# Performance work log

Hardware: AMD Instinct MI355X
Metric: run time of the kernel (lower is better)

Reference implementation:

```python
import jax, jax.numpy as jnp
import numpy as np

N_NODES = 100000
N_EDGES = 1200000
D_IN = 256
D_OUT = 64


def setup_inputs() -> dict:
    key = jax.random.key(0)
    k1, k2, k3, k4, k5 = jax.random.split(key, 5)
    x = jax.random.normal(k1, (N_NODES, D_IN), dtype=jnp.float32)
    edge_row = jax.random.randint(k2, (N_EDGES,), 0, N_NODES, dtype=jnp.int64)
    edge_col = jax.random.randint(k3, (N_EDGES,), 0, N_NODES, dtype=jnp.int64)
    edge_val = jax.random.uniform(k4, (N_EDGES,), dtype=jnp.float32)
    # Xavier-uniform weight, as in reset_parameters()
    limit = float(np.sqrt(6.0 / (D_IN + D_OUT)))
    weight = jax.random.uniform(k5, (D_IN, D_OUT), dtype=jnp.float32,
                                minval=-limit, maxval=limit)
    return {"x": x, "edge_row": edge_row, "edge_col": edge_col,
            "edge_val": edge_val, "weight": weight}


def reference(x, edge_row, edge_col, edge_val, weight):
    # eval mode / dropout p=0.0 -> dropout is identity
    support = x @ weight                               # [N, D_OUT] dense GEMM
    # sparse adjacency spmm: out[i] = sum_{e: row[e]==i} val[e] * support[col[e]]
    msgs = edge_val[:, None] * support[edge_col]       # [E, D_OUT] gather
    out = jax.ops.segment_sum(msgs, edge_row, num_segments=N_NODES)  # scatter-add
    return jax.nn.relu(out)
```

## Files before the change

kernel.cpp:

```cpp
#include <hip/hip_runtime.h>
#include <hip/hip_bf16.h>

#define N_NODES 100000
#define N_EDGES 1200000
#define D_IN 256
#define D_OUT 64
#define N_TILES (N_NODES / 16)

#define NG 1280
#define FUSED_NB (NG * 2)
#define EDGE4_NB ((N_EDGES / 4 + 255) / 256)

#define FILL_PASSES 2
#define PASS_NODES (N_NODES / FILL_PASSES)
#define FILL_NB ((N_EDGES / 4 + 255) / 256)

#define SCAN_BLOCK 1024
#define SCAN_NB ((N_NODES + SCAN_BLOCK - 1) / SCAN_BLOCK)

typedef __bf16 bf16_t;
typedef bf16_t bf16x8 __attribute__((ext_vector_type(8)));
typedef float f32x4 __attribute__((ext_vector_type(4)));

__device__ __forceinline__ unsigned pack_cv(int col, float val) {
    return ((unsigned)col << 15) | (unsigned)(val * 32767.f + 0.5f);
}

__device__ __forceinline__ bf16x8 cvt8(float4 lo, float4 hi) {
    bf16x8 a;
    a[0] = (bf16_t)lo.x; a[1] = (bf16_t)lo.y;
    a[2] = (bf16_t)lo.z; a[3] = (bf16_t)lo.w;
    a[4] = (bf16_t)hi.x; a[5] = (bf16_t)hi.y;
    a[6] = (bf16_t)hi.z; a[7] = (bf16_t)hi.w;
    return a;
}

__device__ __forceinline__ void gld_lds16(const void* g, void* l) {
    __builtin_amdgcn_global_load_lds(
        (const __attribute__((address_space(1))) void*)g,
        (__attribute__((address_space(3))) void*)l, 16, 0, 0);
}

__global__ __launch_bounds__(256) void pack_w(const float* __restrict__ W,
                                              bf16_t* __restrict__ Wpack) {
    int id = blockIdx.x * 256 + threadIdx.x;
    if (id < D_IN * D_OUT) {
        int i  = id & 7;
        int l  = (id >> 3) & 63;
        int n  = (id >> 9) & 3;
        int kk = id >> 11;
        int k = kk * 32 + (l >> 4) * 8 + i;
        int c = n * 16 + (l & 15);
        Wpack[id] = (bf16_t)W[k * D_OUT + c];
    }
}

__device__ __forceinline__ void stage_tile(const char* __restrict__ xtile,
                                           char* ldsbuf, int wave, int lane) {
#pragma unroll
    for (int i = 0; i < 4; ++i) {
        int kk = i * 2 + (wave >> 1);
        const char* src = xtile + (lane & 15) * 1024 + (lane >> 4) * 32
                        + kk * 128 + (wave & 1) * 16;
        gld_lds16(src, ldsbuf + i * 4096 + wave * 1024);
    }
}

__device__ __forceinline__ void compute_store(const char* buf,
                                              const bf16x8* wf,
                                              int lane, int lrow, int g, int wave,
                                              bf16_t* __restrict__ support,
                                              int tile) {
    f32x4 acc = {0.f, 0.f, 0.f, 0.f};
#pragma unroll
    for (int kk = 0; kk < 8; ++kk) {
        float4 lo = *(const float4*)(buf + kk * 2048 + lane * 16);
        float4 hi = *(const float4*)(buf + kk * 2048 + 1024 + lane * 16);
        acc = __builtin_amdgcn_mfma_f32_16x16x32_bf16(cvt8(lo, hi), wf[kk],
                                                      acc, 0, 0, 0);
    }
    bf16_t* __restrict__ sp = support + (size_t)tile * 16 * D_OUT
                            + wave * 16 + lrow;
#pragma unroll
    for (int q = 0; q < 4; ++q)
        sp[(g * 4 + q) * D_OUT] = (bf16_t)acc[q];
}

__global__ __launch_bounds__(256, 5) void gemm_hist_cv(
        const float* __restrict__ x, const bf16x8* __restrict__ Wpack,
        bf16_t* __restrict__ support,
        const int* __restrict__ erow, const int* __restrict__ ecol,
        const float* __restrict__ eval,
        int* __restrict__ counts, unsigned* __restrict__ rcv) {
    __shared__ char xlds[2][16384];
    int bid  = blockIdx.x;
    int role = bid & 1;
    int idx  = bid >> 1;
    if (role == 0) {
        int lane = threadIdx.x & 63;
        int wave = threadIdx.x >> 6;
        int lrow = lane & 15;
        int g    = lane >> 4;

        bf16x8 wf[8];
#pragma unroll
        for (int kk = 0; kk < 8; ++kk)
            wf[kk] = Wpack[(kk * 4 + wave) * 64 + lane];

        const char* xc = (const char*)x;
        int t = idx;
        stage_tile(xc + (size_t)t * 16384, xlds[0], wave, lane);

        int cur = 0;
#pragma unroll 1
        for (; t < N_TILES; t += NG) {
            int nxt = t + NG;
            if (nxt < N_TILES) {
                stage_tile(xc + (size_t)nxt * 16384, xlds[cur ^ 1], wave, lane);
                if (t == idx) {
                    asm volatile("s_waitcnt vmcnt(4)" ::: "memory");
                } else {
                    asm volatile("s_waitcnt vmcnt(8)" ::: "memory");
                }
            } else {
                asm volatile("s_waitcnt vmcnt(4)" ::: "memory");
            }
            __builtin_amdgcn_s_barrier();
            __builtin_amdgcn_sched_barrier(0);
            compute_store(xlds[cur], wf, lane, lrow, g, wave, support, t);
            __builtin_amdgcn_s_barrier();
            __builtin_amdgcn_sched_barrier(0);
            cur ^= 1;
        }
    } else {
        if (idx >= EDGE4_NB) return;
        int e = (idx * 256 + threadIdx.x) * 4;
        if (e + 3 < N_EDGES) {
            int4   r4 = *(const int4*)(erow + e);
            int4   c4 = *(const int4*)(ecol + e);
            float4 v4 = *(const float4*)(eval + e);
            unsigned p0 = (unsigned)atomicAdd(&counts[r4.x], 1);
            unsigned p1 = (unsigned)atomicAdd(&counts[r4.y], 1);
            unsigned p2 = (unsigned)atomicAdd(&counts[r4.z], 1);
            unsigned p3 = (unsigned)atomicAdd(&counts[r4.w], 1);
            uint4 o1, o2;
            o1.x = pack_cv(c4.x, v4.x); o1.y = (unsigned)r4.x | (p0 << 17);
            o1.z = pack_cv(c4.y, v4.y); o1.w = (unsigned)r4.y | (p1 << 17);
            o2.x = pack_cv(c4.z, v4.z); o2.y = (unsigned)r4.z | (p2 << 17);
            o2.z = pack_cv(c4.w, v4.w); o2.w = (unsigned)r4.w | (p3 << 17);
            *(uint4*)(rcv + 2 * e)     = o1;
            *(uint4*)(rcv + 2 * e + 4) = o2;
        } else {
            for (int i = 0; i < 4; ++i) {
                if (e + i < N_EDGES) {
                    int rr = erow[e + i];
                    unsigned pp = (unsigned)atomicAdd(&counts[rr], 1);
                    rcv[2 * (e + i)]     = pack_cv(ecol[e + i], eval[e + i]);
                    rcv[2 * (e + i) + 1] = (unsigned)rr | (pp << 17);
                }
            }
        }
    }
}

__global__ __launch_bounds__(256) void partial_k(const int* __restrict__ counts,
                                                 int* __restrict__ bsum) {
    int b = blockIdx.x, t = threadIdx.x;
    int base = b * SCAN_BLOCK + t * 4;
    int s = 0;
    if (base + 3 < N_NODES) {
        int4 v = *(const int4*)(counts + base);
        s = ((v.x + 3) & ~3) + ((v.y + 3) & ~3) + ((v.z + 3) & ~3) + ((v.w + 3) & ~3);
    } else {
#pragma unroll
        for (int i = 0; i < 4; ++i)
            if (base + i < N_NODES) s += (counts[base + i] + 3) & ~3;
    }
#pragma unroll
    for (int off = 32; off > 0; off >>= 1) s += __shfl_down(s, off);
    __shared__ int sh[4];
    if ((t & 63) == 0) sh[t >> 6] = s;
    __syncthreads();
    if (t == 0) bsum[b] = sh[0] + sh[1] + sh[2] + sh[3];
}

__global__ __launch_bounds__(256) void emit_k(const int* __restrict__ counts,
                                              const int* __restrict__ bsum,
                                              int* __restrict__ offsets) {
    __shared__ int sb[128];
    __shared__ int sh[256];
    int b = blockIdx.x, t = threadIdx.x;
    if (t < 128) sb[t] = (t < SCAN_NB) ? bsum[t] : 0;
    __syncthreads();
    for (int off = 1; off < 128; off <<= 1) {
        int add = (t < 128 && t >= off) ? sb[t - off] : 0;
        __syncthreads();
        if (t < 128) sb[t] += add;
        __syncthreads();
    }
    int bpre = (b == 0) ? 0 : sb[b - 1];

    int base = b * SCAN_BLOCK + t * 4;
    int c0 = 0, c1 = 0, c2 = 0, c3 = 0;
    if (base + 3 < N_NODES) {
        int4 v = *(const int4*)(counts + base);
        c0 = (v.x + 3) & ~3; c1 = (v.y + 3) & ~3;
        c2 = (v.z + 3) & ~3; c3 = (v.w + 3) & ~3;
    } else {
        if (base + 0 < N_NODES) c0 = (counts[base + 0] + 3) & ~3;
        if (base + 1 < N_NODES) c1 = (counts[base + 1] + 3) & ~3;
        if (base + 2 < N_NODES) c2 = (counts[base + 2] + 3) & ~3;
        if (base + 3 < N_NODES) c3 = (counts[base + 3] + 3) & ~3;
    }
    int sum4 = c0 + c1 + c2 + c3;
    sh[t] = sum4;
    __syncthreads();
    for (int off = 1; off < 256; off <<= 1) {
        int add = (t >= off) ? sh[t - off] : 0;
        __syncthreads();
        sh[t] += add;
        __syncthreads();
    }
    int run = bpre + sh[t] - sum4;
    if (base + 0 < N_NODES) { offsets[base + 0] = run; run += c0; }
    if (base + 1 < N_NODES) { offsets[base + 1] = run; run += c1; }
    if (base + 2 < N_NODES) { offsets[base + 2] = run; run += c2; }
    if (base + 3 < N_NODES) { offsets[base + 3] = run; run += c3; }
}

__global__ __launch_bounds__(256) void fill_k(const unsigned* __restrict__ rcv,
                                              const int* __restrict__ offsets,
                                              unsigned* __restrict__ csr,
                                              int lo, int hi) {
    int t = blockIdx.x * 256 + threadIdx.x;
    int e = t * 4;
    if (e + 3 < N_EDGES) {
        uint4 A = *(const uint4*)(rcv + 2 * e);
        uint4 B = *(const uint4*)(rcv + 2 * e + 4);
        int r0 = (int)(A.y & 0x1ffffu), p0 = (int)(A.y >> 17);
        int r1 = (int)(A.w & 0x1ffffu), p1 = (int)(A.w >> 17);
        int r2 = (int)(B.y & 0x1ffffu), p2 = (int)(B.y >> 17);
        int r3 = (int)(B.w & 0x1ffffu), p3 = (int)(B.w >> 17);
        int o0 = offsets[r0];
        int o1 = offsets[r1];
        int o2 = offsets[r2];
        int o3 = offsets[r3];
        if (r0 >= lo && r0 < hi) csr[o0 + p0] = A.x;
        if (r1 >= lo && r1 < hi) csr[o1 + p1] = A.z;
        if (r2 >= lo && r2 < hi) csr[o2 + p2] = B.x;
        if (r3 >= lo && r3 < hi) csr[o3 + p3] = B.z;
    } else {
        for (int i = 0; i < 4; ++i) {
            if (e + i < N_EDGES) {
                unsigned cw = rcv[2 * (e + i)];
                unsigned rw = rcv[2 * (e + i) + 1];
                int rr = (int)(rw & 0x1ffffu);
                int pp = (int)(rw >> 17);
                if (rr >= lo && rr < hi) csr[offsets[rr] + pp] = cw;
            }
        }
    }
}

__global__ __launch_bounds__(256) void agg_k(const int* __restrict__ offsets,
                                             const int* __restrict__ counts,
                                             const unsigned* __restrict__ csr,
                                             const uint2* __restrict__ supq,
                                             float* __restrict__ out) {
    int wave = threadIdx.x >> 6;
    int lane = threadIdx.x & 63;
    int q4   = lane >> 4;
    int fl   = lane & 15;
    int node = blockIdx.x * 16 + wave * 4 + q4;
    if (node >= N_NODES) return;
    int s = offsets[node];
    int e = s + counts[node];
    const float inv = 1.f / 32767.f;
    float a0 = 0.f, a1 = 0.f, a2 = 0.f, a3 = 0.f;
    int p = s;
#define ACC(w, qq) { float v = (float)((w) & 0x7fffu) * inv;                    \
        a0 = fmaf(v, __uint_as_float((qq).x << 16), a0);                        \
        a1 = fmaf(v, __uint_as_float((qq).x & 0xffff0000u), a1);                \
        a2 = fmaf(v, __uint_as_float((qq).y << 16), a2);                        \
        a3 = fmaf(v, __uint_as_float((qq).y & 0xffff0000u), a3); }
    for (; p + 8 <= e; p += 8) {
        uint4 A = *(const uint4*)(csr + p);
        uint4 B = *(const uint4*)(csr + p + 4);
        uint2 q0 = supq[(size_t)(A.x >> 15) * 16 + fl];
        uint2 q1 = supq[(size_t)(A.y >> 15) * 16 + fl];
        uint2 q2 = supq[(size_t)(A.z >> 15) * 16 + fl];
        uint2 q3 = supq[(size_t)(A.w >> 15) * 16 + fl];
        uint2 q4v = supq[(size_t)(B.x >> 15) * 16 + fl];
        uint2 q5 = supq[(size_t)(B.y >> 15) * 16 + fl];
        uint2 q6 = supq[(size_t)(B.z >> 15) * 16 + fl];
        uint2 q7 = supq[(size_t)(B.w >> 15) * 16 + fl];
        ACC(A.x, q0) ACC(A.y, q1) ACC(A.z, q2) ACC(A.w, q3)
        ACC(B.x, q4v) ACC(B.y, q5) ACC(B.z, q6) ACC(B.w, q7)
    }
    if (p + 4 <= e) {
        uint4 A = *(const uint4*)(csr + p);
        uint2 q0 = supq[(size_t)(A.x >> 15) * 16 + fl];
        uint2 q1 = supq[(size_t)(A.y >> 15) * 16 + fl];
        uint2 q2 = supq[(size_t)(A.z >> 15) * 16 + fl];
        uint2 q3 = supq[(size_t)(A.w >> 15) * 16 + fl];
        ACC(A.x, q0) ACC(A.y, q1) ACC(A.z, q2) ACC(A.w, q3)
        p += 4;
    }
    for (; p < e; ++p) {
        unsigned w = csr[p];
        uint2 q = supq[(size_t)(w >> 15) * 16 + fl];
        ACC(w, q)
    }
#undef ACC
    float4 r;
    r.x = fmaxf(a0, 0.f);
    r.y = fmaxf(a1, 0.f);
    r.z = fmaxf(a2, 0.f);
    r.w = fmaxf(a3, 0.f);
    *(float4*)(out + (size_t)node * D_OUT + fl * 4) = r;
}

extern "C" void kernel_launch(void* const* d_in, const int* in_sizes, int n_in,
                              void* d_out, int out_size, void* d_ws, size_t ws_size,
                              hipStream_t stream) {
    const float* x    = (const float*)d_in[0];
    const int*   erow = (const int*)d_in[1];
    const int*   ecol = (const int*)d_in[2];
    const float* eval = (const float*)d_in[3];
    const float* W    = (const float*)d_in[4];
    float* out = (float*)d_out;

    char* ws = (char*)d_ws;
    bf16_t*   support = (bf16_t*)ws;
    bf16_t*   WpackS  = (bf16_t*)(ws + 12800000);
    int*      counts  = (int*)(ws + 12832768);
    int*      offsets = (int*)(ws + 13232768);
    unsigned* rcv     = (unsigned*)(ws + 13632784);
    unsigned* csr     = (unsigned*)(ws + 23232784);
    int*      bsum    = (int*)(ws + 29232784);

    pack_w<<<(D_IN * D_OUT + 255) / 256, 256, 0, stream>>>(W, WpackS);

    hipMemsetAsync(counts, 0, (size_t)N_NODES * sizeof(int), stream);
    gemm_hist_cv<<<FUSED_NB, 256, 0, stream>>>(
        x, (const bf16x8*)WpackS, support, erow, ecol, eval, counts, rcv);

    partial_k<<<SCAN_NB, 256, 0, stream>>>(counts, bsum);
    emit_k<<<SCAN_NB, 256, 0, stream>>>(counts, bsum, offsets);

    for (int p = 0; p < FILL_PASSES; ++p) {
        fill_k<<<FILL_NB, 256, 0, stream>>>(rcv, offsets, csr,
                                            p * PASS_NODES, (p + 1) * PASS_NODES);
    }

    agg_k<<<(N_NODES + 15) / 16, 256, 0, stream>>>(offsets, counts, csr,
                                                   (const uint2*)support, out);
}
```

Measured before the change: 121.6 us.

## Replace persistent double-buffered GEMM blocks with one-tile-per-block grid interleaved with histogram

The fused GEMM+histogram kernel drops its persistent, double-buffered loop over tiles and instead launches one block per 16-row tile, interleaving 5 GEMM blocks with 1 edge-histogram block in each group of 6. LDS use is halved to a single buffer and launch bounds are raised to allow 8 blocks per CU, so latency is hidden by occupancy rather than explicit prefetch. In exchange, every block reloads the packed weight fragments and pays its own launch and sync cost, with no overlap of load and compute inside a block.

```diff
diff --git a/kernel.cpp b/kernel.cpp
--- a/kernel.cpp
+++ b/kernel.cpp
@@ -7,8 +7,8 @@
 #define D_OUT 64
 #define N_TILES (N_NODES / 16)
 
-#define NG 1280
-#define FUSED_NB (NG * 2)
+#define FUSED_PERIODS 1250
+#define FUSED_NB (FUSED_PERIODS * 6)
 #define EDGE4_NB ((N_EDGES / 4 + 255) / 256)
 
 #define FILL_PASSES 2
@@ -86,55 +86,34 @@
         sp[(g * 4 + q) * D_OUT] = (bf16_t)acc[q];
 }
 
-__global__ __launch_bounds__(256, 5) void gemm_hist_cv(
+__global__ __launch_bounds__(256, 8) void gemm_hist_cv(
         const float* __restrict__ x, const bf16x8* __restrict__ Wpack,
         bf16_t* __restrict__ support,
         const int* __restrict__ erow, const int* __restrict__ ecol,
         const float* __restrict__ eval,
         int* __restrict__ counts, unsigned* __restrict__ rcv) {
-    __shared__ char xlds[2][16384];
-    int bid  = blockIdx.x;
-    int role = bid & 1;
-    int idx  = bid >> 1;
-    if (role == 0) {
+    __shared__ char xlds[16384];
+    int p = blockIdx.x / 6;
+    int r = blockIdx.x % 6;
+    if (r < 5) {
+        int t = p * 5 + r;
         int lane = threadIdx.x & 63;
         int wave = threadIdx.x >> 6;
         int lrow = lane & 15;
         int g    = lane >> 4;
 
+        stage_tile((const char*)x + (size_t)t * 16384, xlds, wave, lane);
+
         bf16x8 wf[8];
 #pragma unroll
         for (int kk = 0; kk < 8; ++kk)
             wf[kk] = Wpack[(kk * 4 + wave) * 64 + lane];
 
-        const char* xc = (const char*)x;
-        int t = idx;
-        stage_tile(xc + (size_t)t * 16384, xlds[0], wave, lane);
-
-        int cur = 0;
-#pragma unroll 1
-        for (; t < N_TILES; t += NG) {
-            int nxt = t + NG;
-            if (nxt < N_TILES) {
-                stage_tile(xc + (size_t)nxt * 16384, xlds[cur ^ 1], wave, lane);
-                if (t == idx) {
-                    asm volatile("s_waitcnt vmcnt(4)" ::: "memory");
-                } else {
-                    asm volatile("s_waitcnt vmcnt(8)" ::: "memory");
-                }
-            } else {
-                asm volatile("s_waitcnt vmcnt(4)" ::: "memory");
-            }
-            __builtin_amdgcn_s_barrier();
-            __builtin_amdgcn_sched_barrier(0);
-            compute_store(xlds[cur], wf, lane, lrow, g, wave, support, t);
-            __builtin_amdgcn_s_barrier();
-            __builtin_amdgcn_sched_barrier(0);
-            cur ^= 1;
-        }
+        __syncthreads();
+        compute_store(xlds, wf, lane, lrow, g, wave, support, t);
     } else {
-        if (idx >= EDGE4_NB) return;
-        int e = (idx * 256 + threadIdx.x) * 4;
+        if (p >= EDGE4_NB) return;
+        int e = (p * 256 + threadIdx.x) * 4;
         if (e + 3 < N_EDGES) {
             int4   r4 = *(const int4*)(erow + e);
             int4   c4 = *(const int4*)(ecol + e);
```

Result: slower. 124.5 us (+2.4%).

## Merge scan kernels with redundant prefix sums and fill CSR in one pass

Applied to the files above, without the earlier changes.

Two changes. The two-kernel prefix scan (partial block sums, then emit) becomes one kernel where each block recomputes the sum of all earlier counts itself, which removes a launch and the bsum round trip but adds redundant reads, quadratic in the block count. The CSR fill, previously two row-range passes over the edge list (likely there to keep scattered writes cache-local), now runs as one pass with no range checks. That halves reads of rcv and offsets and drops a launch, at the risk of less cache-friendly scattered writes.

```diff
diff --git a/kernel.cpp b/kernel.cpp
--- a/kernel.cpp
+++ b/kernel.cpp
@@ -10,9 +10,6 @@
 #define NG 1280
 #define FUSED_NB (NG * 2)
 #define EDGE4_NB ((N_EDGES / 4 + 255) / 256)
-
-#define FILL_PASSES 2
-#define PASS_NODES (N_NODES / FILL_PASSES)
 #define FILL_NB ((N_EDGES / 4 + 255) / 256)
 
 #define SCAN_BLOCK 1024
@@ -163,42 +160,24 @@
     }
 }
 
-__global__ __launch_bounds__(256) void partial_k(const int* __restrict__ counts,
-                                                 int* __restrict__ bsum) {
+__global__ __launch_bounds__(256) void scan_emit_k(const int* __restrict__ counts,
+                                                   int* __restrict__ offsets) {
+    __shared__ int sh[256];
+    __shared__ int sw[4];
     int b = blockIdx.x, t = threadIdx.x;
-    int base = b * SCAN_BLOCK + t * 4;
-    int s = 0;
-    if (base + 3 < N_NODES) {
+
+    int limit = b * SCAN_BLOCK;
+    int pre = 0;
+    for (int base = t * 4; base + 3 < limit; base += 1024) {
         int4 v = *(const int4*)(counts + base);
-        s = ((v.x + 3) & ~3) + ((v.y + 3) & ~3) + ((v.z + 3) & ~3) + ((v.w + 3) & ~3);
-    } else {
-#pragma unroll
-        for (int i = 0; i < 4; ++i)
-            if (base + i < N_NODES) s += (counts[base + i] + 3) & ~3;
-    }
-#pragma unroll
-    for (int off = 32; off > 0; off >>= 1) s += __shfl_down(s, off);
-    __shared__ int sh[4];
-    if ((t & 63) == 0) sh[t >> 6] = s;
+        pre += ((v.x + 3) & ~3) + ((v.y + 3) & ~3)
+             + ((v.z + 3) & ~3) + ((v.w + 3) & ~3);
+    }
+#pragma unroll
+    for (int off = 32; off > 0; off >>= 1) pre += __shfl_down(pre, off);
+    if ((t & 63) == 0) sw[t >> 6] = pre;
     __syncthreads();
-    if (t == 0) bsum[b] = sh[0] + sh[1] + sh[2] + sh[3];
-}
-
-__global__ __launch_bounds__(256) void emit_k(const int* __restrict__ counts,
-                                              const int* __restrict__ bsum,
-                                              int* __restrict__ offsets) {
-    __shared__ int sb[128];
-    __shared__ int sh[256];
-    int b = blockIdx.x, t = threadIdx.x;
-    if (t < 128) sb[t] = (t < SCAN_NB) ? bsum[t] : 0;
-    __syncthreads();
-    for (int off = 1; off < 128; off <<= 1) {
-        int add = (t < 128 && t >= off) ? sb[t - off] : 0;
-        __syncthreads();
-        if (t < 128) sb[t] += add;
-        __syncthreads();
-    }
-    int bpre = (b == 0) ? 0 : sb[b - 1];
+    int bpre = sw[0] + sw[1] + sw[2] + sw[3];
 
     int base = b * SCAN_BLOCK + t * 4;
     int c0 = 0, c1 = 0, c2 = 0, c3 = 0;
@@ -230,8 +209,7 @@
 
 __global__ __launch_bounds__(256) void fill_k(const unsigned* __restrict__ rcv,
                                               const int* __restrict__ offsets,
-                                              unsigned* __restrict__ csr,
-                                              int lo, int hi) {
+                                              unsigned* __restrict__ csr) {
     int t = blockIdx.x * 256 + threadIdx.x;
     int e = t * 4;
     if (e + 3 < N_EDGES) {
@@ -245,10 +223,10 @@
         int o1 = offsets[r1];
         int o2 = offsets[r2];
         int o3 = offsets[r3];
-        if (r0 >= lo && r0 < hi) csr[o0 + p0] = A.x;
-        if (r1 >= lo && r1 < hi) csr[o1 + p1] = A.z;
-        if (r2 >= lo && r2 < hi) csr[o2 + p2] = B.x;
-        if (r3 >= lo && r3 < hi) csr[o3 + p3] = B.z;
+        csr[o0 + p0] = A.x;
+        csr[o1 + p1] = A.z;
+        csr[o2 + p2] = B.x;
+        csr[o3 + p3] = B.z;
     } else {
         for (int i = 0; i < 4; ++i) {
             if (e + i < N_EDGES) {
@@ -256,7 +234,7 @@
                 unsigned rw = rcv[2 * (e + i) + 1];
                 int rr = (int)(rw & 0x1ffffu);
                 int pp = (int)(rw >> 17);
-                if (rr >= lo && rr < hi) csr[offsets[rr] + pp] = cw;
+                csr[offsets[rr] + pp] = cw;
             }
         }
     }
@@ -337,7 +315,6 @@
     int*      offsets = (int*)(ws + 13232768);
     unsigned* rcv     = (unsigned*)(ws + 13632784);
     unsigned* csr     = (unsigned*)(ws + 23232784);
-    int*      bsum    = (int*)(ws + 29232784);
 
     pack_w<<<(D_IN * D_OUT + 255) / 256, 256, 0, stream>>>(W, WpackS);
 
@@ -345,13 +322,9 @@
     gemm_hist_cv<<<FUSED_NB, 256, 0, stream>>>(
         x, (const bf16x8*)WpackS, support, erow, ecol, eval, counts, rcv);
 
-    partial_k<<<SCAN_NB, 256, 0, stream>>>(counts, bsum);
-    emit_k<<<SCAN_NB, 256, 0, stream>>>(counts, bsum, offsets);
-
-    for (int p = 0; p < FILL_PASSES; ++p) {
-        fill_k<<<FILL_NB, 256, 0, stream>>>(rcv, offsets, csr,
-                                            p * PASS_NODES, (p + 1) * PASS_NODES);
-    }
+    scan_emit_k<<<SCAN_NB, 256, 0, stream>>>(counts, offsets);
+
+    fill_k<<<FILL_NB, 256, 0, stream>>>(rcv, offsets, csr);
 
     agg_k<<<(N_NODES + 15) / 16, 256, 0, stream>>>(offsets, counts, csr,
                                                    (const uint2*)support, out);
```

Result: slower. 131.2 us (+7.9%).
